# Performance work log

Hardware: AMD Instinct MI355X
Metric: run time of the kernel (lower is better)

The kernel has to match this reference:

```python
import jax, jax.numpy as jnp
import numpy as np

B, N, E, D = 4, 4096, 4096, 128
NEG_SLOPE = 0.01
BN_EPS = 1e-5


def setup_inputs() -> dict:
    key = jax.random.key(0)
    ks = jax.random.split(key, 8)
    return {
        "incident_mat": (jax.random.uniform(ks[0], (B, N, E)) < 0.01).astype(jnp.float32),
        "degree_v": jax.random.normal(ks[1], (B, N, N), jnp.float32) * 0.01,
        "degree_e": jax.random.normal(ks[2], (B, E, E), jnp.float32) * 0.01,
        "x": jax.random.normal(ks[3], (B, N, D), jnp.float32),
        "e_masks": jax.random.randint(ks[4], (B, E), 0, 2, jnp.int32),
        "mlp_W": jax.random.normal(ks[5], (D, D), jnp.float32) / np.sqrt(D),
        "mlp_b": jnp.zeros((D,), jnp.float32),
        "theta_att": jax.random.normal(ks[6], (D, 1), jnp.float32) / np.sqrt(D),
        "eps": jax.random.uniform(ks[7], (1,), jnp.float32),
        "bn_gamma": jnp.ones((D,), jnp.float32),
        "bn_beta": jnp.zeros((D,), jnp.float32),
        "bn_mean": jnp.zeros((D,), jnp.float32),
        "bn_var": jnp.ones((D,), jnp.float32),
    }


def reference(incident_mat, degree_v, degree_e, x, e_masks, mlp_W, mlp_b,
              theta_att, eps, bn_gamma, bn_beta, bn_mean, bn_var):
    # MLP (num_mlp_layers=1 -> single Linear)
    x_w = x @ mlp_W + mlp_b                      # [B,N,D]
    Ht = jnp.swapaxes(incident_mat, 1, 2)        # [B,E,N]
    ht_x_w = Ht @ x_w                            # [B,E,D]
    # attention logits per hyperedge
    ht_x_theta = (Ht @ (x @ theta_att))[..., 0]  # [B,E]
    scores = jnp.where(e_masks == 0, -jnp.inf, ht_x_theta)
    attn = jax.nn.softmax(scores, axis=1)        # [B,E]
    # diag_embed + bmm == elementwise row scaling
    h1 = attn[..., None] * ht_x_w                # [B,E,D]
    h1 = incident_mat @ h1                       # [B,N,D]
    h1 = degree_v @ h1                           # [B,N,D]
    h1 = Ht @ h1                                 # [B,E,D]
    h1 = degree_e @ h1                           # [B,E,D]
    h = h1 + eps * ht_x_w                        # [B,E,D]
    h = incident_mat @ h                         # [B,N,D]
    h = jnp.where(h >= 0, h, NEG_SLOPE * h)      # leaky_relu; dropout=identity (eval)
    # BatchNorm1d over channels (inference mode)
    h = (h - bn_mean) / jnp.sqrt(bn_var + BN_EPS) * bn_gamma + bn_beta
    return h
```

## Files before the change

### kernel.cpp

```cpp
#include <hip/hip_runtime.h>


typedef __bf16 bf16;
typedef bf16 bf16x8 __attribute__((ext_vector_type(8)));
typedef float f32x4 __attribute__((ext_vector_type(4)));
typedef unsigned long long u64;
typedef unsigned short u16;
typedef u16 u16x8 __attribute__((ext_vector_type(8)));

#define LDK 72
#define LDM 136
#define SWZ(r, c) ((c) ^ ((((r) >> 3) & 7) << 3))
#define CAP 192

union BPack { bf16 h[2]; unsigned int u; };
static __device__ __forceinline__ bf16 tob(float f) { return (bf16)f; }

__global__ __launch_bounds__(256) void mlp_k(const float* __restrict__ x,
                                             const float* __restrict__ W,
                                             const float* __restrict__ bias,
                                             const float* __restrict__ theta,
                                             float* __restrict__ xw,
                                             float* __restrict__ xt) {
    __shared__ __align__(16) bf16 Xs[64][LDM];
    __shared__ __align__(16) bf16 Ws[128][LDM];
    const int t = threadIdx.x;
    const long r0 = (long)blockIdx.x * 64;

    {
        const int row = t >> 2, c = (t & 3) * 32;
        const float* g = x + (r0 + row) * 128 + c;
#pragma unroll
        for (int j8 = 0; j8 < 4; ++j8) {
            float4 v0 = *(const float4*)(g + j8 * 8);
            float4 v1 = *(const float4*)(g + j8 * 8 + 4);
            bf16x8 p;
            p[0] = tob(v0.x); p[1] = tob(v0.y); p[2] = tob(v0.z); p[3] = tob(v0.w);
            p[4] = tob(v1.x); p[5] = tob(v1.y); p[6] = tob(v1.z); p[7] = tob(v1.w);
            *(bf16x8*)&Xs[row][c + j8 * 8] = p;
        }
    }
    {
        const int wk = t >> 1, wh = (t & 1) * 64;
        const float* g = W + wk * 128 + wh;
#pragma unroll
        for (int j = 0; j < 64; j += 4) {
            float4 v = *(const float4*)(g + j);
            Ws[wh + j + 0][wk] = tob(v.x);
            Ws[wh + j + 1][wk] = tob(v.y);
            Ws[wh + j + 2][wk] = tob(v.z);
            Ws[wh + j + 3][wk] = tob(v.w);
        }
    }
    __syncthreads();

    const int wave = t >> 6, lane = t & 63;
    const int lr = lane & 15, kb = lane >> 4;
    const int wm = wave * 16;

    f32x4 acc[8];
#pragma unroll
    for (int ct = 0; ct < 8; ++ct) acc[ct] = (f32x4){0.f, 0.f, 0.f, 0.f};

#pragma unroll
    for (int step = 0; step < 4; ++step) {
        const int ka = step * 32 + kb * 8;
        bf16x8 af = *(const bf16x8*)&Xs[wm + lr][ka];
#pragma unroll
        for (int ct = 0; ct < 8; ++ct) {
            bf16x8 bfr = *(const bf16x8*)&Ws[ct * 16 + lr][ka];
            acc[ct] = __builtin_amdgcn_mfma_f32_16x16x32_bf16(af, bfr, acc[ct], 0, 0, 0);
        }
    }

    {
        const int row = t >> 2, q = t & 3;
        float p = 0.f;
#pragma unroll
        for (int kk = 0; kk < 32; ++kk)
            p += (float)Xs[row][q * 32 + kk] * theta[q * 32 + kk];
        p += __shfl_down(p, 2);
        p += __shfl_down(p, 1);
        if (q == 0) xt[r0 + row] = p;
    }

#pragma unroll
    for (int ct = 0; ct < 8; ++ct) {
        const int col = ct * 16 + lr;
        const float bd = bias[col];
#pragma unroll
        for (int i = 0; i < 4; ++i)
            xw[(r0 + wm + kb * 4 + i) * 128 + col] = acc[ct][i] + bd;
    }
}

__global__ __launch_bounds__(256) void bmask_lists_k(const float* __restrict__ inc,
                                                     u64* __restrict__ rowmask,
                                                     u16* __restrict__ idx,
                                                     int* __restrict__ cnts) {
    const int b = blockIdx.y;
    const int n = blockIdx.x * 4 + (threadIdx.x >> 6);
    const int l = threadIdx.x & 63;
    const float* p = inc + ((long)b << 24) + (long)n * 4096 + l * 64;
    u64 w = 0;
#pragma unroll
    for (int j = 0; j < 16; ++j) {
        const float4 v = *(const float4*)(p + j * 4);
        w |= (u64)(v.x != 0.f ? 1u : 0u) << (4 * j);
        w |= (u64)(v.y != 0.f ? 1u : 0u) << (4 * j + 1);
        w |= (u64)(v.z != 0.f ? 1u : 0u) << (4 * j + 2);
        w |= (u64)(v.w != 0.f ? 1u : 0u) << (4 * j + 3);
    }
    const long rowid = (long)b * 4096 + n;
    rowmask[rowid * 64 + l] = w;

    const int pc = __popcll(w);
    int pre = pc;
#pragma unroll
    for (int o = 1; o < 64; o <<= 1) {
        int t = __shfl_up(pre, o);
        if (l >= o) pre += t;
    }
    if (l == 63) cnts[rowid] = pre;
    u16* op = idx + rowid * CAP;
    int k = pre - pc;
    u64 m = w;
    while (m) {
        const int bit = __builtin_ctzll(m);
        m &= m - 1;
        if (k < CAP) op[k] = (u16)(l * 64 + bit);
        ++k;
    }
}

__global__ __launch_bounds__(64) void btrans_lists_k(const u64* __restrict__ rowmask,
                                                     u64* __restrict__ colmask,
                                                     u16* __restrict__ idx,
                                                     int* __restrict__ cnts) {
    const int te = blockIdx.x, b = blockIdx.y;
    const int l = threadIdx.x;
    __shared__ u64 w[64];
    const long rowid = (long)b * 4096 + te * 64 + l;
    u16* op = idx + rowid * CAP;
    int k = 0;

    u64 nx = rowmask[((long)b * 4096 + l) * 64 + te];
    for (int tn = 0; tn < 64; ++tn) {
        w[l] = nx;
        __syncthreads();
        if (tn < 63) nx = rowmask[((long)b * 4096 + (tn + 1) * 64 + l) * 64 + te];
        u64 o = 0;
#pragma unroll 8
        for (int j = 0; j < 64; ++j) o |= ((w[j] >> l) & 1ull) << j;
        colmask[rowid * 64 + tn] = o;
        while (o) {
            const int bit = __builtin_ctzll(o);
            o &= o - 1;
            if (k < CAP) op[k] = (u16)(tn * 64 + bit);
            ++k;
        }
        __syncthreads();
    }
    cnts[rowid] = k;
}

__global__ void softmax_k(const float* __restrict__ sc, const int* __restrict__ mask,
                          float* __restrict__ attn) {
    const int b = blockIdx.x, t = threadIdx.x;
    __shared__ float red[1024];
    const float* sb = sc + b * 4096;
    const int* mb = mask + b * 4096;

    float mx = -1e30f;
    for (int e = t; e < 4096; e += 1024)
        if (mb[e] != 0) mx = fmaxf(mx, sb[e]);
    red[t] = mx;
    __syncthreads();
    for (int st = 512; st > 0; st >>= 1) {
        if (t < st) red[t] = fmaxf(red[t], red[t + st]);
        __syncthreads();
    }
    mx = red[0];
    __syncthreads();

    float sum = 0.f;
    for (int e = t; e < 4096; e += 1024)
        if (mb[e] != 0) sum += expf(sb[e] - mx);
    red[t] = sum;
    __syncthreads();
    for (int st = 512; st > 0; st >>= 1) {
        if (t < st) red[t] += red[t + st];
        __syncthreads();
    }
    const float inv = 1.f / red[0];
    for (int e = t; e < 4096; e += 1024)
        attn[b * 4096 + e] = (mb[e] != 0) ? expf(sb[e] - mx) * inv : 0.f;
}

__global__ __launch_bounds__(256) void scale_k(const float* __restrict__ hxw,
                                               const float* __restrict__ att,
                                               float* __restrict__ outp) {
    const long i4 = (long)blockIdx.x * 256 + threadIdx.x;
    float4 v = ((const float4*)hxw)[i4];
    const float s = att[i4 >> 5];
    v.x *= s; v.y *= s; v.z *= s; v.w *= s;
    ((float4*)outp)[i4] = v;
}

template <int KSP, bool EPS>
__global__ __launch_bounds__(256) void pairsum_k(const float* __restrict__ P,
                                                 const float* __restrict__ H,
                                                 const float* __restrict__ epsp,
                                                 float* __restrict__ O) {
    const long i4 = (long)blockIdx.x * 256 + threadIdx.x;
    float4 a = ((const float4*)P)[i4];
#pragma unroll
    for (int s = 1; s < KSP; ++s) {
        float4 c = ((const float4*)P)[i4 + (long)s * 524288];
        a.x += c.x; a.y += c.y; a.z += c.z; a.w += c.w;
    }
    if (EPS) {
        const float e = epsp[0];
        float4 h = ((const float4*)H)[i4];
        a.x += e * h.x; a.y += e * h.y; a.z += e * h.z; a.w += e * h.w;
    }
    ((float4*)O)[i4] = a;
}

template <bool HXT, bool EPI>
__global__ __launch_bounds__(256) void gatherE_k(
    const u16* __restrict__ idx, const int* __restrict__ cnts,
    const u64* __restrict__ mask, const float* __restrict__ src,
    const float* __restrict__ xt,
    const float* __restrict__ bng, const float* __restrict__ bnb,
    const float* __restrict__ bnm, const float* __restrict__ bnv,
    float* __restrict__ out, float* __restrict__ hxt) {
    const int bid = blockIdx.x;
    const int slot = bid & 7;
    const int b = slot >> 1;
    const int chunk = (bid >> 3) * 2 + (slot & 1);
    const int r = chunk * 4 + (threadIdx.x >> 6);
    const int l = threadIdx.x & 63;
    const long rowid = (long)b * 4096 + r;
    const int cnt = cnts[rowid];
    const u16* ip = idx + rowid * CAP;
    const float* S = src + (long)b * 524288;
    const float* xb = xt + (long)b * 4096;
    const int c0 = 2 * l;

    float ax0 = 0.f, ax1 = 0.f, ax2 = 0.f, ax3 = 0.f;
    float ax4 = 0.f, ax5 = 0.f, ax6 = 0.f, ax7 = 0.f;
    float ay0 = 0.f, ay1 = 0.f, ay2 = 0.f, ay3 = 0.f;
    float ay4 = 0.f, ay5 = 0.f, ay6 = 0.f, ay7 = 0.f;
    float hacc = 0.f;

    const int n = cnt < CAP ? cnt : CAP;
    int i = 0;
    if (n >= 8) {
        u16x8 ia = *(const u16x8*)ip;
        for (; i + 8 <= n; i += 8) {
            const int e0 = ia[0], e1 = ia[1], e2 = ia[2], e3 = ia[3];
            const int e4 = ia[4], e5 = ia[5], e6 = ia[6], e7 = ia[7];
            const float2 v0 = *(const float2*)(S + (long)e0 * 128 + c0);
            const float2 v1 = *(const float2*)(S + (long)e1 * 128 + c0);
            const float2 v2 = *(const float2*)(S + (long)e2 * 128 + c0);
            const float2 v3 = *(const float2*)(S + (long)e3 * 128 + c0);
            const float2 v4 = *(const float2*)(S + (long)e4 * 128 + c0);
            const float2 v5 = *(const float2*)(S + (long)e5 * 128 + c0);
            const float2 v6 = *(const float2*)(S + (long)e6 * 128 + c0);
            const float2 v7 = *(const float2*)(S + (long)e7 * 128 + c0);
            const bool more = (i + 16 <= n);
            u16x8 ib;
            if (more) ib = *(const u16x8*)(ip + i + 8);
            if (HXT)
                hacc += ((xb[e0] + xb[e1]) + (xb[e2] + xb[e3])) +
                        ((xb[e4] + xb[e5]) + (xb[e6] + xb[e7]));
            ax0 += v0.x; ay0 += v0.y; ax1 += v1.x; ay1 += v1.y;
            ax2 += v2.x; ay2 += v2.y; ax3 += v3.x; ay3 += v3.y;
            ax4 += v4.x; ay4 += v4.y; ax5 += v5.x; ay5 += v5.y;
            ax6 += v6.x; ay6 += v6.y; ax7 += v7.x; ay7 += v7.y;
            if (more) ia = ib;
        }
    }
    for (; i < n; ++i) {
        const int e = ip[i];
        const float2 v = *(const float2*)(S + (long)e * 128 + c0);
        if (HXT) hacc += xb[e];
        ax0 += v.x; ay0 += v.y;
    }

    if (cnt > CAP) {
        const u64 wrd = mask[rowid * 64 + l];
        int seen = 0;
        for (int wi = 0; wi < 64; ++wi) {
            u64 m = __shfl(wrd, wi);
            const int pc = __popcll(m);
            if (seen + pc > CAP) {
                int tk = CAP - seen;
                if (tk < 0) tk = 0;
                for (int t = 0; t < tk; ++t) m &= m - 1;
                while (m) {
                    const int bit = __builtin_ctzll(m);
                    m &= m - 1;
                    const int e = (wi << 6) + bit;
                    const float2 v = *(const float2*)(S + (long)e * 128 + c0);
                    if (HXT) hacc += xb[e];
                    ax0 += v.x; ay0 += v.y;
                }
            }
            seen += pc;
        }
    }

    float ax = ((ax0 + ax1) + (ax2 + ax3)) + ((ax4 + ax5) + (ax6 + ax7));
    float ay = ((ay0 + ay1) + (ay2 + ay3)) + ((ay4 + ay5) + (ay6 + ay7));
    if (EPI) {
        float t0 = (ax >= 0.f) ? ax : 0.01f * ax;
        float t1 = (ay >= 0.f) ? ay : 0.01f * ay;
        ax = (t0 - bnm[c0]) * rsqrtf(bnv[c0] + 1e-5f) * bng[c0] + bnb[c0];
        ay = (t1 - bnm[c0 + 1]) * rsqrtf(bnv[c0 + 1] + 1e-5f) * bng[c0 + 1] + bnb[c0 + 1];
    }
    *(float2*)&out[(long)b * 524288 + (long)r * 128 + c0] = (float2){ax, ay};
    if (HXT && l == 0) hxt[rowid] = hacc;
}

template <int KS>
__global__ __launch_bounds__(1024, 4) void gemm_dense(
    const float* __restrict__ A, const float* __restrict__ Bsrc,
    float* __restrict__ P) {
    __shared__ __align__(16) bf16 As[2][128][LDK];
    __shared__ __align__(16) bf16 Bs[2][128][LDK];

    const int tid = threadIdx.x;
    const int bid = blockIdx.x;
    const int slot = bid & 7;
    const int b = slot >> 1;
    const int sub = (bid >> 3) * 2 + (slot & 1);
    const int ksi = sub % KS;
    const int m0 = (sub / KS) * 128;
    constexpr int KCH = 4096 / KS;
    const int kbeg = ksi * KCH, kend = kbeg + KCH;
    const long Aoff = (long)b << 24;
    const long Boff = (long)b * 524288;

    const int wave = tid >> 6, lane = tid & 63;
    const int lr = lane & 15, kb = lane >> 4;
    const int wm = (wave >> 2) * 32, wn = (wave & 3) * 32;

    const int ar = tid >> 3, ak = (tid & 7) * 8;
    const int bd4 = (tid & 31) * 4, bk2 = (tid >> 5) * 2;

    const float* Abase = A + Aoff + (long)(m0 + ar) * 4096 + ak;
    const float* Bbase = Bsrc + Boff + (long)bk2 * 128 + bd4;

    f32x4 acc[2][2];
#pragma unroll
    for (int mf = 0; mf < 2; ++mf)
#pragma unroll
        for (int nf = 0; nf < 2; ++nf) acc[mf][nf] = (f32x4){0.f, 0.f, 0.f, 0.f};

    float4 pa0A, pa1A, pb0A, pb1A;
    float4 pa0B, pa1B, pb0B, pb1B;

#define GLOAD(S, kk)                                                        \
    {                                                                       \
        const float* ga = Abase + (kk);                                     \
        pa0##S = *(const float4*)ga;                                        \
        pa1##S = *(const float4*)(ga + 4);                                  \
        const float* gb = Bbase + (long)(kk) * 128;                         \
        pb0##S = *(const float4*)gb;                                        \
        pb1##S = *(const float4*)(gb + 128);                                \
    }

#define STAGE(S, bu)                                                        \
    {                                                                       \
        bf16x8 p;                                                           \
        p[0] = tob(pa0##S.x); p[1] = tob(pa0##S.y); p[2] = tob(pa0##S.z); p[3] = tob(pa0##S.w); \
        p[4] = tob(pa1##S.x); p[5] = tob(pa1##S.y); p[6] = tob(pa1##S.z); p[7] = tob(pa1##S.w); \
        *(bf16x8*)&As[bu][ar][SWZ(ar, ak)] = p;                             \
        float va[4] = {pb0##S.x, pb0##S.y, pb0##S.z, pb0##S.w};             \
        float vb[4] = {pb1##S.x, pb1##S.y, pb1##S.z, pb1##S.w};             \
        _Pragma("unroll")                                                   \
        for (int j = 0; j < 4; ++j) {                                       \
            BPack q; q.h[0] = tob(va[j]); q.h[1] = tob(vb[j]);              \
            *(unsigned int*)&Bs[bu][bd4 + j][SWZ(bd4 + j, bk2)] = q.u;      \
        }                                                                   \
    }

#define MFMA_STEP(bu)                                                       \
    {                                                                       \
        _Pragma("unroll")                                                   \
        for (int ks = 0; ks < 2; ++ks) {                                    \
            const int ka = ks * 32 + kb * 8;                                \
            bf16x8 af[2], bfr[2];                                           \
            _Pragma("unroll")                                               \
            for (int mf = 0; mf < 2; ++mf) {                                \
                const int rA = wm + mf * 16 + lr;                           \
                af[mf] = *(const bf16x8*)&As[bu][rA][SWZ(rA, ka)];          \
            }                                                               \
            _Pragma("unroll")                                               \
            for (int nf = 0; nf < 2; ++nf) {                                \
                const int rB = wn + nf * 16 + lr;                           \
                bfr[nf] = *(const bf16x8*)&Bs[bu][rB][SWZ(rB, ka)];         \
            }                                                               \
            _Pragma("unroll")                                               \
            for (int mf = 0; mf < 2; ++mf)                                  \
                _Pragma("unroll")                                           \
                for (int nf = 0; nf < 2; ++nf)                              \
                    acc[mf][nf] = __builtin_amdgcn_mfma_f32_16x16x32_bf16(  \
                        af[mf], bfr[nf], acc[mf][nf], 0, 0, 0);             \
        }                                                                   \
    }

    GLOAD(A, kbeg);
    GLOAD(B, kbeg + 64);
    STAGE(A, 0);
    __syncthreads();

    for (int kk = kbeg; kk < kend; kk += 128) {
        MFMA_STEP(0);
        STAGE(B, 1);
        if (kk + 128 < kend) GLOAD(A, kk + 128);
        __syncthreads();
        MFMA_STEP(1);
        if (kk + 128 < kend) {
            STAGE(A, 0);
            if (kk + 192 < kend) GLOAD(B, kk + 192);
            __syncthreads();
        }
    }
#undef GLOAD
#undef STAGE
#undef MFMA_STEP

    float* Cp = P + (long)(ksi * 4 + b) * 524288;
#pragma unroll
    for (int mf = 0; mf < 2; ++mf) {
        const int rb = m0 + wm + mf * 16 + kb * 4;
#pragma unroll
        for (int nf = 0; nf < 2; ++nf) {
            const int col = wn + nf * 16 + lr;
#pragma unroll
            for (int i = 0; i < 4; ++i)
                Cp[(long)(rb + i) * 128 + col] = acc[mf][nf][i];
        }
    }
}

template <int KS>
static void run_all(const float* incident, const float* degree_v, const float* degree_e,
                    const float* x, const int* e_masks, const float* mlp_W,
                    const float* mlp_b, const float* theta, const float* epsp,
                    const float* bng, const float* bnb, const float* bnm,
                    const float* bnv, float* out, float* ws, hipStream_t stream) {
    float* xw    = ws;
    float* hxw   = ws + 2097152;
    float* hxw_s = ws + 4194304;
    float* t1    = ws + 6291456;
    float* Pd    = ws + 8388608;
    float* Psum  = Pd + (long)KS * 2097152;
    float* tail  = Psum + 2097152;
    u64* rowmask = (u64*)tail;
    u64* colmask = rowmask + 1048576;
    u16* rowidx = (u16*)(colmask + 1048576);
    u16* colidx = rowidx + 16384 * CAP;
    int* rowcnt = (int*)(colidx + 16384 * CAP);
    int* colcnt = rowcnt + 16384;
    float* xt  = (float*)(colcnt + 16384);
    float* hxt = xt + 16384;
    float* att = hxt + 16384;

    mlp_k<<<256, 256, 0, stream>>>(x, mlp_W, mlp_b, theta, xw, xt);
    bmask_lists_k<<<dim3(1024, 4), 256, 0, stream>>>(incident, rowmask, rowidx, rowcnt);
    btrans_lists_k<<<dim3(64, 4), 64, 0, stream>>>(rowmask, colmask, colidx, colcnt);

    gatherE_k<true, false><<<4096, 256, 0, stream>>>(
        colidx, colcnt, colmask, xw, xt, nullptr, nullptr, nullptr, nullptr,
        hxw, hxt);
    softmax_k<<<4, 1024, 0, stream>>>(hxt, e_masks, att);
    scale_k<<<2048, 256, 0, stream>>>(hxw, att, hxw_s);
    gatherE_k<false, false><<<4096, 256, 0, stream>>>(
        rowidx, rowcnt, rowmask, hxw_s, xt, nullptr, nullptr, nullptr, nullptr,
        t1, nullptr);
    gemm_dense<KS><<<32 * KS * 4, 1024, 0, stream>>>(degree_v, t1, Pd);
    pairsum_k<KS, false><<<2048, 256, 0, stream>>>(Pd, nullptr, nullptr, Psum);
    gatherE_k<false, false><<<4096, 256, 0, stream>>>(
        colidx, colcnt, colmask, Psum, xt, nullptr, nullptr, nullptr, nullptr,
        t1, nullptr);
    gemm_dense<KS><<<32 * KS * 4, 1024, 0, stream>>>(degree_e, t1, Pd);
    pairsum_k<KS, true><<<2048, 256, 0, stream>>>(Pd, hxw, epsp, Psum);
    gatherE_k<false, true><<<4096, 256, 0, stream>>>(
        rowidx, rowcnt, rowmask, Psum, xt, bng, bnb, bnm, bnv, out, nullptr);
}

extern "C" void kernel_launch(void* const* d_in, const int* in_sizes, int n_in,
                              void* d_out, int out_size, void* d_ws, size_t ws_size,
                              hipStream_t stream) {
    const float* incident = (const float*)d_in[0];
    const float* degree_v = (const float*)d_in[1];
    const float* degree_e = (const float*)d_in[2];
    const float* x        = (const float*)d_in[3];
    const int*   e_masks  = (const int*)d_in[4];
    const float* mlp_W    = (const float*)d_in[5];
    const float* mlp_b    = (const float*)d_in[6];
    const float* theta    = (const float*)d_in[7];
    const float* epsp     = (const float*)d_in[8];
    const float* bng      = (const float*)d_in[9];
    const float* bnb      = (const float*)d_in[10];
    const float* bnm      = (const float*)d_in[11];
    const float* bnv      = (const float*)d_in[12];
    float* out = (float*)d_out;
    float* ws = (float*)d_ws;

    if (ws_size >= 110000000ull)
        run_all<2>(incident, degree_v, degree_e, x, e_masks, mlp_W, mlp_b, theta,
                   epsp, bng, bnb, bnm, bnv, out, ws, stream);
    else
        run_all<1>(incident, degree_v, degree_e, x, e_masks, mlp_W, mlp_b, theta,
                   epsp, bng, bnb, bnm, bnv, out, ws, stream);
}
```

Baseline: 443.4 us.

## Split bitmask transpose and column-list build into parallel kernels

The old transpose kernel ran only 256 single-wave blocks, each walking 64 tiles in sequence and building column index lists serially per thread. It is replaced by a fully parallel transpose kernel with one block per 64x64 tile, plus a separate list-building kernel that uses a wave-wide prefix sum over popcounts, like the row-list kernel. The goal is to remove a serial, low-occupancy stage from the critical path, at the cost of one more launch and an extra read of the column mask.

Result: faster. 385.4 us (-13.1%).

```diff
diff --git a/kernel.cpp b/kernel.cpp
--- a/kernel.cpp
+++ b/kernel.cpp
@@ -133,35 +133,41 @@
     }
 }
 
-__global__ __launch_bounds__(64) void btrans_lists_k(const u64* __restrict__ rowmask,
-                                                     u64* __restrict__ colmask,
-                                                     u16* __restrict__ idx,
-                                                     int* __restrict__ cnts) {
-    const int te = blockIdx.x, b = blockIdx.y;
+__global__ void btrans_k(const u64* __restrict__ rowmask, u64* __restrict__ colmask) {
+    const int tn = blockIdx.x, te = blockIdx.y, b = blockIdx.z;
     const int l = threadIdx.x;
     __shared__ u64 w[64];
-    const long rowid = (long)b * 4096 + te * 64 + l;
-    u16* op = idx + rowid * CAP;
-    int k = 0;
-
-    u64 nx = rowmask[((long)b * 4096 + l) * 64 + te];
-    for (int tn = 0; tn < 64; ++tn) {
-        w[l] = nx;
-        __syncthreads();
-        if (tn < 63) nx = rowmask[((long)b * 4096 + (tn + 1) * 64 + l) * 64 + te];
-        u64 o = 0;
+    w[l] = rowmask[((long)b * 4096 + tn * 64 + l) * 64 + te];
+    __syncthreads();
+    u64 o = 0;
 #pragma unroll 8
-        for (int j = 0; j < 64; ++j) o |= ((w[j] >> l) & 1ull) << j;
-        colmask[rowid * 64 + tn] = o;
-        while (o) {
-            const int bit = __builtin_ctzll(o);
-            o &= o - 1;
-            if (k < CAP) op[k] = (u16)(tn * 64 + bit);
-            ++k;
-        }
-        __syncthreads();
-    }
-    cnts[rowid] = k;
+    for (int j = 0; j < 64; ++j) o |= ((w[j] >> l) & 1ull) << j;
+    colmask[((long)b * 4096 + te * 64 + l) * 64 + tn] = o;
+}
+
+__global__ __launch_bounds__(256) void lists_k(const u64* __restrict__ mask,
+                                               u16* __restrict__ idx,
+                                               int* __restrict__ cnts) {
+    const int b = blockIdx.y;
+    const int r = blockIdx.x * 4 + (threadIdx.x >> 6);
+    const int l = threadIdx.x & 63;
+    u64 m = mask[((long)b * 4096 + r) * 64 + l];
+    const int pc = __popcll(m);
+    int pre = pc;
+#pragma unroll
+    for (int o = 1; o < 64; o <<= 1) {
+        int t = __shfl_up(pre, o);
+        if (l >= o) pre += t;
+    }
+    if (l == 63) cnts[b * 4096 + r] = pre;
+    u16* op = idx + ((long)b * 4096 + r) * CAP;
+    int k = pre - pc;
+    while (m) {
+        const int bit = __builtin_ctzll(m);
+        m &= m - 1;
+        if (k < CAP) op[k] = (u16)(l * 64 + bit);
+        ++k;
+    }
 }
 
 __global__ void softmax_k(const float* __restrict__ sc, const int* __restrict__ mask,
@@ -472,7 +478,8 @@
 
     mlp_k<<<256, 256, 0, stream>>>(x, mlp_W, mlp_b, theta, xw, xt);
     bmask_lists_k<<<dim3(1024, 4), 256, 0, stream>>>(incident, rowmask, rowidx, rowcnt);
-    btrans_lists_k<<<dim3(64, 4), 64, 0, stream>>>(rowmask, colmask, colidx, colcnt);
+    btrans_k<<<dim3(64, 64, 4), 64, 0, stream>>>(rowmask, colmask);
+    lists_k<<<dim3(1024, 4), 256, 0, stream>>>(colmask, colidx, colcnt);
 
     gatherE_k<true, false><<<4096, 256, 0, stream>>>(
         colidx, colcnt, colmask, xw, xt, nullptr, nullptr, nullptr, nullptr,
```
